# Kernel optimization log

Hardware: AMD Instinct MI355X
Metric: run time of the kernel (lower is better)

Reference implementation:

```python
import jax, jax.numpy as jnp
import numpy as np

D_IN = 1024
D_OUT = 1024
N, S = 4, 2048

def setup_inputs() -> dict:
    key = jax.random.key(0)
    kv, kk, kq, k1, k2, k3 = jax.random.split(key, 6)
    return {
        "v": jax.random.normal(kv, (N, S, D_IN), dtype=jnp.float32),
        "k": jax.random.normal(kk, (N, S, D_IN), dtype=jnp.float32),
        "q": jax.random.normal(kq, (N, S, D_IN), dtype=jnp.float32),
        "WV": jax.random.normal(k1, (D_OUT, D_IN), dtype=jnp.float32),
        "WQ": jax.random.normal(k2, (D_OUT, D_IN), dtype=jnp.float32),
        "WK": jax.random.normal(k3, (D_OUT, D_IN), dtype=jnp.float32),
    }

def reference(v, k, q, WV, WQ, WK) -> jnp.ndarray:
    # projections: x @ W.T  -> [N, S, D_OUT]
    wv = jnp.einsum('nsw,ow->nso', v, WV)
    wk = jnp.einsum('nsw,ow->nso', k, WK)
    wq = jnp.einsum('nsw,ow->nso', q, WQ)
    # scores [N, Sq, Sk]; NOTE: softmax over axis=1 (query axis, matching torch dim=1),
    # then post-hoc division by input_shape[0] AFTER softmax (faithful to source).
    scores = jnp.einsum('nqo,nko->nqk', wq, wk)
    wqk = jax.nn.softmax(scores, axis=1) / jnp.float32(D_IN)
    return jnp.einsum('nqk,nko->nqo', wqk, wv)
```

## Files before the change

### kernel.cpp

```cpp
#include <hip/hip_runtime.h>
#include <math.h>


typedef _Float16 f16;
typedef _Float16 f16x8 __attribute__((ext_vector_type(8)));
typedef _Float16 f16x4 __attribute__((ext_vector_type(4)));
typedef float f32x4 __attribute__((ext_vector_type(4)));

enum StageMode { SM_PLANES2, SM_PLANES1 };
enum EpiMode   { EPI_F32, EPI_SPLIT, EPI_F16T };

#define GLL_PITCH 32

__device__ __forceinline__ void gll16(const f16* g, f16* l) {
    __builtin_amdgcn_global_load_lds(
        (const __attribute__((address_space(1))) void*)g,
        (__attribute__((address_space(3))) void*)l, 16, 0, 0);
}

__device__ __forceinline__ void stage_gll_plane(const f16* __restrict__ gplane,
                                                f16* __restrict__ lds,
                                                long rowBase, int ld, int k0,
                                                int wave, int lane)
{
#pragma unroll
    for (int i = 0; i < 2; i++) {
        int slotBase = (wave * 2 + i) * 64;
        int t = slotBase + lane;
        int r = t >> 2;
        int c = (t & 3) ^ ((r >> 1) & 3);
        const f16* g = gplane + (rowBase + r) * (long)ld + k0 + c * 8;
        gll16(g, lds + (long)slotBase * 8);
    }
}

__device__ __forceinline__ int frag_off_gll(int row, int g) {
    return row * GLL_PITCH + ((g ^ ((row >> 1) & 3)) << 3);
}

template<StageMode SA, StageMode SB, EpiMode EP, int GROUPM, bool STATS>
__global__ __launch_bounds__(256, 4)
void mfma_gemm(const f16* __restrict__ Ahi, const f16* __restrict__ Alo,
               const f16* __restrict__ Bhi, const f16* __restrict__ Blo,
               float* __restrict__ pmOut, float* __restrict__ psOut,
               void* __restrict__ C0, void* __restrict__ C1,
               int M, int Nc, int K, int lda, int ldb, int ldc,
               long batchA, long batchB, long batchC,
               float epiScale, int tsShift)
{
    constexpr bool TRIPLE = (SA == SM_PLANES2);
    constexpr int PLANE_SZ = 128 * GLL_PITCH;

    int bx, by;
    if constexpr (GROUPM > 0) {
        int gx = gridDim.x;
        int lin = blockIdx.y * gx + blockIdx.x;
        int nig = GROUPM * gx;
        int gid = lin / nig;
        int rem = lin - gid * nig;
        by = gid * GROUPM + (rem % GROUPM);
        bx = rem / GROUPM;
    } else {
        bx = blockIdx.x;
        by = blockIdx.y;
    }
    const int n0 = bx * 128;
    const int m0 = by * 128;
    const long z = blockIdx.z;

    const long aOfs = z * batchA, bOfs = z * batchB, cOfs = z * batchC;

    __shared__ __align__(16) f16 As_hi[PLANE_SZ];
    __shared__ __align__(16) f16 Bs_hi[PLANE_SZ];
    __shared__ __align__(16) f16 As_lo[TRIPLE ? PLANE_SZ : 8];
    __shared__ __align__(16) f16 Bs_lo[TRIPLE ? PLANE_SZ : 8];

    const int tid  = threadIdx.x;
    const int lane = tid & 63;
    const int wave = tid >> 6;
    const int wr = (wave >> 1) * 64;
    const int wc = (wave & 1) * 64;
    const int fm = lane & 15;
    const int fg = lane >> 4;

    f32x4 acc[4][4];
#pragma unroll
    for (int i = 0; i < 4; i++)
#pragma unroll
        for (int j = 0; j < 4; j++) acc[i][j] = (f32x4){0.f, 0.f, 0.f, 0.f};

    int roA[4], roB[4];
#pragma unroll
    for (int i = 0; i < 4; i++) {
        roA[i] = frag_off_gll(wr + i * 16 + fm, fg);
        roB[i] = frag_off_gll(wc + i * 16 + fm, fg);
    }

    for (int k0 = 0; k0 < K; k0 += 32) {
        stage_gll_plane(Ahi + aOfs, As_hi, m0, lda, k0, wave, lane);
        stage_gll_plane(Bhi + bOfs, Bs_hi, n0, ldb, k0, wave, lane);
        if constexpr (TRIPLE) {
            stage_gll_plane(Alo + aOfs, As_lo, m0, lda, k0, wave, lane);
            stage_gll_plane(Blo + bOfs, Bs_lo, n0, ldb, k0, wave, lane);
        }
        __syncthreads();

        f16x8 ah[4], bh[4], al[4], bl[4];
#pragma unroll
        for (int i = 0; i < 4; i++) {
            ah[i] = *(const f16x8*)&As_hi[roA[i]];
            bh[i] = *(const f16x8*)&Bs_hi[roB[i]];
            if constexpr (TRIPLE) {
                al[i] = *(const f16x8*)&As_lo[roA[i]];
                bl[i] = *(const f16x8*)&Bs_lo[roB[i]];
            }
        }
#pragma unroll
        for (int i = 0; i < 4; i++) {
#pragma unroll
            for (int j = 0; j < 4; j++) {
                acc[i][j] = __builtin_amdgcn_mfma_f32_16x16x32_f16(ah[i], bh[j], acc[i][j], 0, 0, 0);
                if constexpr (TRIPLE) {
                    acc[i][j] = __builtin_amdgcn_mfma_f32_16x16x32_f16(ah[i], bl[j], acc[i][j], 0, 0, 0);
                    acc[i][j] = __builtin_amdgcn_mfma_f32_16x16x32_f16(al[i], bh[j], acc[i][j], 0, 0, 0);
                }
            }
        }
        __syncthreads();
    }

    const int cr = fg * 4;
    const int cn = fm;
#pragma unroll
    for (int i = 0; i < 4; i++) {
#pragma unroll
        for (int j = 0; j < 4; j++) {
#pragma unroll
            for (int r = 0; r < 4; r++) {
                long mg = m0 + wr + i * 16 + cr + r;
                long ng = n0 + wc + j * 16 + cn;
                float val = acc[i][j][r] * epiScale;
                if constexpr (EP == EPI_F32) {
                    ((float*)C0)[cOfs + mg * ldc + ng] = val;
                } else if constexpr (EP == EPI_SPLIT) {
                    f16 h = (f16)val;
                    ((f16*)C0)[cOfs + mg * ldc + ng] = h;
                    ((f16*)C1)[cOfs + mg * ldc + ng] = (f16)(val - (float)h);
                } else {
                    long TS = 1L << tsShift;
                    long nb = mg >> tsShift;
                    long s  = mg & (TS - 1);
                    long addr = nb * ((long)Nc << tsShift) + ng * TS + s;
                    ((f16*)C0)[addr] = (f16)val;
                }
            }
        }
    }

    if constexpr (STATS) {
        __shared__ float stM[2][128];
        __shared__ float stS[2][128];
#pragma unroll
        for (int j = 0; j < 4; j++) {
            float mj = -3.402823466e38f;
#pragma unroll
            for (int i = 0; i < 4; i++)
#pragma unroll
                for (int r = 0; r < 4; r++) mj = fmaxf(mj, acc[i][j][r]);
            float sj = 0.f;
#pragma unroll
            for (int i = 0; i < 4; i++)
#pragma unroll
                for (int r = 0; r < 4; r++) sj += __expf(acc[i][j][r] - mj);
#pragma unroll
            for (int mask = 16; mask <= 32; mask <<= 1) {
                float mo = __shfl_xor(mj, mask, 64);
                float so = __shfl_xor(sj, mask, 64);
                float mn = fmaxf(mj, mo);
                sj = sj * __expf(mj - mn) + so * __expf(mo - mn);
                mj = mn;
            }
            if (fg == 0) {
                stM[wave >> 1][wc + j * 16 + cn] = mj;
                stS[wave >> 1][wc + j * 16 + cn] = sj;
            }
        }
        __syncthreads();
        if (tid < 128) {
            float ma = stM[0][tid], mb = stM[1][tid];
            float Mc = fmaxf(ma, mb);
            float Sv = stS[0][tid] * __expf(ma - Mc) + stS[1][tid] * __expf(mb - Mc);
            long o = ((long)z * (M >> 7) + by) * (long)Nc + (long)bx * 128 + tid;
            pmOut[o] = Mc;
            psOut[o] = Sv;
        }
    }
}

template<bool HAS_LO>
__global__ __launch_bounds__(256)
void split_kernel(const float* __restrict__ src, f16* __restrict__ hi,
                  f16* __restrict__ lo, long n)
{
    long i = ((long)blockIdx.x * 256 + threadIdx.x) * 8;
    if (i >= n) return;
    float4 x0 = *(const float4*)&src[i];
    float4 x1 = *(const float4*)&src[i + 4];
    float xs[8] = {x0.x, x0.y, x0.z, x0.w, x1.x, x1.y, x1.z, x1.w};
    f16x8 h, l;
#pragma unroll
    for (int e = 0; e < 8; e++) {
        f16 hh = (f16)xs[e];
        h[e] = hh;
        if (HAS_LO) l[e] = (f16)(xs[e] - (float)hh);
    }
    *(f16x8*)&hi[i] = h;
    if (HAS_LO) *(f16x8*)&lo[i] = l;
}

__global__ __launch_bounds__(64)
void stats_combine_kernel(const float* __restrict__ pm, const float* __restrict__ ps,
                          float* __restrict__ statM, float* __restrict__ statR, int S)
{
    const int n = blockIdx.y;
    const int kk = blockIdx.x * 64 + threadIdx.x;
    float M = -INFINITY;
#pragma unroll
    for (int i = 0; i < 16; i++)
        M = fmaxf(M, pm[((long)n * 16 + i) * S + kk]);
    float Ssum = 0.f;
#pragma unroll
    for (int i = 0; i < 16; i++)
        Ssum += ps[((long)n * 16 + i) * S + kk] * __expf(pm[((long)n * 16 + i) * S + kk] - M);
    statM[(long)n * S + kk] = M;
    statR[(long)n * S + kk] = 1.0f / Ssum;
}

__global__ __launch_bounds__(256)
void pmat_kernel(const float* __restrict__ Sc, const float* __restrict__ statM,
                 const float* __restrict__ statR, f16* __restrict__ Phi, int S)
{
    const int n = blockIdx.z;
    const int kk = blockIdx.x * 1024 + threadIdx.x * 4;
    const float* Sn = Sc + (long)n * S * S;
    f16* ph = Phi + (long)n * S * S;
    float4 M4 = *(const float4*)&statM[(long)n * S + kk];
    float4 R4 = *(const float4*)&statR[(long)n * S + kk];
    const int q0 = blockIdx.y * 32;
    for (int qi = 0; qi < 32; qi++) {
        long idx = (long)(q0 + qi) * S + kk;
        float4 x = *(const float4*)&Sn[idx];
        f16x4 p;
        p[0] = (f16)(__expf(x.x - M4.x) * R4.x);
        p[1] = (f16)(__expf(x.y - M4.y) * R4.y);
        p[2] = (f16)(__expf(x.z - M4.z) * R4.z);
        p[3] = (f16)(__expf(x.w - M4.w) * R4.w);
        *(f16x4*)&ph[idx] = p;
    }
}

extern "C" void kernel_launch(void* const* d_in, const int* in_sizes, int n_in,
                              void* d_out, int out_size, void* d_ws, size_t ws_size,
                              hipStream_t stream)
{
    const float* v  = (const float*)d_in[0];
    const float* k  = (const float*)d_in[1];
    const float* q  = (const float*)d_in[2];
    const float* WV = (const float*)d_in[3];
    const float* WQ = (const float*)d_in[4];
    const float* WK = (const float*)d_in[5];
    float* out = (float*)d_out;

    const int N = 4, S = 2048, D = 1024;
    const long NSD = (long)N * S * D;
    const long DD  = (long)D * D;

    f16* ws = (f16*)d_ws;
    f16* q_hi = ws;
    f16* q_lo = ws + NSD;
    f16* k_hi = ws + 2 * NSD;
    f16* k_lo = ws + 3 * NSD;
    f16* v_hi = ws + 4 * NSD;
    f16* Wb   = ws + 5 * NSD;
    f16* WQ_hi = Wb,          *WQ_lo = Wb + DD;
    f16* WK_hi = Wb + 2 * DD, *WK_lo = Wb + 3 * DD;
    f16* WV_hi = Wb + 4 * DD;
    f16* wq_hi = ws + 5 * NSD + 5 * DD;
    f16* wq_lo = wq_hi + NSD;
    f16* wk_hi = wq_hi + 2 * NSD;
    f16* wk_lo = wq_hi + 3 * NSD;
    f16* wvT_hi = ws;
    float* Sc   = (float*)(ws + NSD);
    f16* P_hi   = wq_hi;
    float* pm    = (float*)(ws + 9 * NSD + 5 * DD);
    float* ps    = pm + (long)N * 16 * S;
    float* statM = ps + (long)N * 16 * S;
    float* statR = statM + (long)N * S;

    dim3 blk(256);

    split_kernel<true ><<<dim3(NSD / 2048), blk, 0, stream>>>(q,  q_hi, q_lo, NSD);
    split_kernel<true ><<<dim3(NSD / 2048), blk, 0, stream>>>(k,  k_hi, k_lo, NSD);
    split_kernel<false><<<dim3(NSD / 2048), blk, 0, stream>>>(v,  v_hi, nullptr, NSD);
    split_kernel<true ><<<dim3(DD / 2048),  blk, 0, stream>>>(WQ, WQ_hi, WQ_lo, DD);
    split_kernel<true ><<<dim3(DD / 2048),  blk, 0, stream>>>(WK, WK_hi, WK_lo, DD);
    split_kernel<false><<<dim3(DD / 2048),  blk, 0, stream>>>(WV, WV_hi, nullptr, DD);

    {
        dim3 g(D / 128, (N * S) / 128, 1);
        mfma_gemm<SM_PLANES2, SM_PLANES2, EPI_SPLIT, 4, false><<<g, blk, 0, stream>>>(
            q_hi, q_lo, WQ_hi, WQ_lo, nullptr, nullptr, wq_hi, wq_lo,
            N * S, D, D, D, D, D, 0, 0, 0, 1.0f, 0);
        mfma_gemm<SM_PLANES2, SM_PLANES2, EPI_SPLIT, 4, false><<<g, blk, 0, stream>>>(
            k_hi, k_lo, WK_hi, WK_lo, nullptr, nullptr, wk_hi, wk_lo,
            N * S, D, D, D, D, D, 0, 0, 0, 1.0f, 0);
        mfma_gemm<SM_PLANES1, SM_PLANES1, EPI_F16T, 4, false><<<g, blk, 0, stream>>>(
            v_hi, nullptr, WV_hi, nullptr, nullptr, nullptr, wvT_hi, nullptr,
            N * S, D, D, D, D, 0, 0, 0, 0, 1.0f, 11 );
    }
    {
        dim3 g(S / 128, S / 128, N);
        mfma_gemm<SM_PLANES2, SM_PLANES2, EPI_F32, 4, true><<<g, blk, 0, stream>>>(
            wq_hi, wq_lo, wk_hi, wk_lo, pm, ps, Sc, nullptr,
            S, S, D, D, D, S, (long)S * D, (long)S * D, (long)S * S, 1.0f, 0);
    }
    {
        dim3 gB(S / 64, N);
        stats_combine_kernel<<<gB, dim3(64), 0, stream>>>(pm, ps, statM, statR, S);
    }
    {
        dim3 g(S / 1024, S / 32, N);
        pmat_kernel<<<g, blk, 0, stream>>>(Sc, statM, statR, P_hi, S);
    }
    {
        dim3 g(D / 128, S / 128, N);
        mfma_gemm<SM_PLANES1, SM_PLANES1, EPI_F32, 4, false><<<g, blk, 0, stream>>>(
            P_hi, nullptr, wvT_hi, nullptr, nullptr, nullptr, out, nullptr,
            S, D, S, S, S, D, (long)S * S, (long)S * D, (long)S * D, 1.0f / (float)D, 0);
    }
}
```

Baseline: 471.8 us.

## Fuse softmax normalization into PV GEMM A-load and merge split kernels

Removes the separate pmat kernel by having the final GEMM stage fp32 scores into LDS and apply exp(x-M)*R with an f16 conversion in registers while building A fragments. This avoids writing and re-reading the f16 probability matrix, but each of the 8 column tiles now rereads fp32 scores and recomputes the exponentials. The six split launches are also merged into two launches. The fused GEMM uses launch bounds of 2 blocks and no group swizzle, because of the larger LDS footprint and register use.

```diff
diff --git a/kernel.cpp b/kernel.cpp
--- a/kernel.cpp
+++ b/kernel.cpp
@@ -4,15 +4,14 @@
 
 typedef _Float16 f16;
 typedef _Float16 f16x8 __attribute__((ext_vector_type(8)));
-typedef _Float16 f16x4 __attribute__((ext_vector_type(4)));
 typedef float f32x4 __attribute__((ext_vector_type(4)));
 
-enum StageMode { SM_PLANES2, SM_PLANES1 };
+enum StageMode { SM_PLANES2, SM_PLANES1, SM_EXPF32 };
 enum EpiMode   { EPI_F32, EPI_SPLIT, EPI_F16T };
 
 #define GLL_PITCH 32
 
-__device__ __forceinline__ void gll16(const f16* g, f16* l) {
+__device__ __forceinline__ void gll16(const void* g, void* l) {
     __builtin_amdgcn_global_load_lds(
         (const __attribute__((address_space(1))) void*)g,
         (__attribute__((address_space(3))) void*)l, 16, 0, 0);
@@ -34,14 +33,31 @@
     }
 }
 
+__device__ __forceinline__ void stage_gll_f32(const float* __restrict__ gplane,
+                                              float* __restrict__ lds,
+                                              long rowBase, int ld, int k0,
+                                              int wave, int lane)
+{
+#pragma unroll
+    for (int i = 0; i < 4; i++) {
+        int slotBase = (wave * 4 + i) * 64;
+        int t = slotBase + lane;
+        int r = t >> 3;
+        int lc = (t & 7) ^ (r & 7);
+        const float* g = gplane + (rowBase + r) * (long)ld + k0 + lc * 4;
+        gll16(g, lds + (long)slotBase * 4);
+    }
+}
+
 __device__ __forceinline__ int frag_off_gll(int row, int g) {
     return row * GLL_PITCH + ((g ^ ((row >> 1) & 3)) << 3);
 }
 
-template<StageMode SA, StageMode SB, EpiMode EP, int GROUPM, bool STATS>
-__global__ __launch_bounds__(256, 4)
-void mfma_gemm(const f16* __restrict__ Ahi, const f16* __restrict__ Alo,
-               const f16* __restrict__ Bhi, const f16* __restrict__ Blo,
+template<StageMode SA, StageMode SB, EpiMode EP, int GROUPM, bool STATS, int LB>
+__global__ __launch_bounds__(256, LB)
+void mfma_gemm(const void* __restrict__ Ahi, const void* __restrict__ Alo,
+               const void* __restrict__ Bhi, const void* __restrict__ Blo,
+               const float* __restrict__ statM, const float* __restrict__ statR,
                float* __restrict__ pmOut, float* __restrict__ psOut,
                void* __restrict__ C0, void* __restrict__ C1,
                int M, int Nc, int K, int lda, int ldb, int ldc,
@@ -50,6 +66,7 @@
 {
     constexpr bool TRIPLE = (SA == SM_PLANES2);
     constexpr int PLANE_SZ = 128 * GLL_PITCH;
+    constexpr bool A_F32 = (SA == SM_EXPF32);
 
     int bx, by;
     if constexpr (GROUPM > 0) {
@@ -70,7 +87,7 @@
 
     const long aOfs = z * batchA, bOfs = z * batchB, cOfs = z * batchC;
 
-    __shared__ __align__(16) f16 As_hi[PLANE_SZ];
+    __shared__ __align__(16) f16 As_hi[A_F32 ? 2 * PLANE_SZ : PLANE_SZ];
     __shared__ __align__(16) f16 Bs_hi[PLANE_SZ];
     __shared__ __align__(16) f16 As_lo[TRIPLE ? PLANE_SZ : 8];
     __shared__ __align__(16) f16 Bs_lo[TRIPLE ? PLANE_SZ : 8];
@@ -97,23 +114,55 @@
     }
 
     for (int k0 = 0; k0 < K; k0 += 32) {
-        stage_gll_plane(Ahi + aOfs, As_hi, m0, lda, k0, wave, lane);
-        stage_gll_plane(Bhi + bOfs, Bs_hi, n0, ldb, k0, wave, lane);
-        if constexpr (TRIPLE) {
-            stage_gll_plane(Alo + aOfs, As_lo, m0, lda, k0, wave, lane);
-            stage_gll_plane(Blo + bOfs, Bs_lo, n0, ldb, k0, wave, lane);
-        }
+        if constexpr (A_F32) {
+            stage_gll_f32((const float*)Ahi + aOfs, (float*)As_hi, m0, lda, k0, wave, lane);
+        } else {
+            stage_gll_plane((const f16*)Ahi + aOfs, As_hi, m0, lda, k0, wave, lane);
+            if constexpr (TRIPLE)
+                stage_gll_plane((const f16*)Alo + aOfs, As_lo, m0, lda, k0, wave, lane);
+        }
+        stage_gll_plane((const f16*)Bhi + bOfs, Bs_hi, n0, ldb, k0, wave, lane);
+        if constexpr (TRIPLE)
+            stage_gll_plane((const f16*)Blo + bOfs, Bs_lo, n0, ldb, k0, wave, lane);
         __syncthreads();
 
         f16x8 ah[4], bh[4], al[4], bl[4];
+        if constexpr (A_F32) {
+            const float* pM = statM + z * (long)K;
+            const float* pR = statR + z * (long)K;
+            float4 Ma = *(const float4*)&pM[k0 + fg * 8];
+            float4 Mb = *(const float4*)&pM[k0 + fg * 8 + 4];
+            float4 Ra = *(const float4*)&pR[k0 + fg * 8];
+            float4 Rb = *(const float4*)&pR[k0 + fg * 8 + 4];
+            const float* Asf = (const float*)As_hi;
+            const int p0 = (fg << 1) ^ (fm & 7);
+#pragma unroll
+            for (int i = 0; i < 4; i++) {
+                int ra = wr + i * 16 + fm;
+                float4 xa = *(const float4*)&Asf[ra * 32 + p0 * 4];
+                float4 xb = *(const float4*)&Asf[ra * 32 + (p0 ^ 1) * 4];
+                f16x8 h;
+                h[0] = (f16)(__expf(xa.x - Ma.x) * Ra.x);
+                h[1] = (f16)(__expf(xa.y - Ma.y) * Ra.y);
+                h[2] = (f16)(__expf(xa.z - Ma.z) * Ra.z);
+                h[3] = (f16)(__expf(xa.w - Ma.w) * Ra.w);
+                h[4] = (f16)(__expf(xb.x - Mb.x) * Rb.x);
+                h[5] = (f16)(__expf(xb.y - Mb.y) * Rb.y);
+                h[6] = (f16)(__expf(xb.z - Mb.z) * Rb.z);
+                h[7] = (f16)(__expf(xb.w - Mb.w) * Rb.w);
+                ah[i] = h;
+            }
+        } else {
+#pragma unroll
+            for (int i = 0; i < 4; i++) {
+                ah[i] = *(const f16x8*)&As_hi[roA[i]];
+                if constexpr (TRIPLE) al[i] = *(const f16x8*)&As_lo[roA[i]];
+            }
+        }
 #pragma unroll
         for (int i = 0; i < 4; i++) {
-            ah[i] = *(const f16x8*)&As_hi[roA[i]];
             bh[i] = *(const f16x8*)&Bs_hi[roB[i]];
-            if constexpr (TRIPLE) {
-                al[i] = *(const f16x8*)&As_lo[roA[i]];
-                bl[i] = *(const f16x8*)&Bs_lo[roB[i]];
-            }
+            if constexpr (TRIPLE) bl[i] = *(const f16x8*)&Bs_lo[roB[i]];
         }
 #pragma unroll
         for (int i = 0; i < 4; i++) {
@@ -197,11 +246,17 @@
     }
 }
 
-template<bool HAS_LO>
 __global__ __launch_bounds__(256)
-void split_kernel(const float* __restrict__ src, f16* __restrict__ hi,
-                  f16* __restrict__ lo, long n)
-{
+void split3_kernel(const float* __restrict__ s0, const float* __restrict__ s1,
+                   const float* __restrict__ s2,
+                   f16* __restrict__ h0, f16* __restrict__ l0,
+                   f16* __restrict__ h1, f16* __restrict__ l1,
+                   f16* __restrict__ h2, long n)
+{
+    const int which = blockIdx.y;
+    const float* src = which == 0 ? s0 : which == 1 ? s1 : s2;
+    f16* hi = which == 0 ? h0 : which == 1 ? h1 : h2;
+    f16* lo = which == 0 ? l0 : which == 1 ? l1 : nullptr;
     long i = ((long)blockIdx.x * 256 + threadIdx.x) * 8;
     if (i >= n) return;
     float4 x0 = *(const float4*)&src[i];
@@ -212,10 +267,10 @@
     for (int e = 0; e < 8; e++) {
         f16 hh = (f16)xs[e];
         h[e] = hh;
-        if (HAS_LO) l[e] = (f16)(xs[e] - (float)hh);
+        l[e] = (f16)(xs[e] - (float)hh);
     }
     *(f16x8*)&hi[i] = h;
-    if (HAS_LO) *(f16x8*)&lo[i] = l;
+    if (lo) *(f16x8*)&lo[i] = l;
 }
 
 __global__ __launch_bounds__(64)
@@ -234,29 +289,6 @@
         Ssum += ps[((long)n * 16 + i) * S + kk] * __expf(pm[((long)n * 16 + i) * S + kk] - M);
     statM[(long)n * S + kk] = M;
     statR[(long)n * S + kk] = 1.0f / Ssum;
-}
-
-__global__ __launch_bounds__(256)
-void pmat_kernel(const float* __restrict__ Sc, const float* __restrict__ statM,
-                 const float* __restrict__ statR, f16* __restrict__ Phi, int S)
-{
-    const int n = blockIdx.z;
-    const int kk = blockIdx.x * 1024 + threadIdx.x * 4;
-    const float* Sn = Sc + (long)n * S * S;
-    f16* ph = Phi + (long)n * S * S;
-    float4 M4 = *(const float4*)&statM[(long)n * S + kk];
-    float4 R4 = *(const float4*)&statR[(long)n * S + kk];
-    const int q0 = blockIdx.y * 32;
-    for (int qi = 0; qi < 32; qi++) {
-        long idx = (long)(q0 + qi) * S + kk;
-        float4 x = *(const float4*)&Sn[idx];
-        f16x4 p;
-        p[0] = (f16)(__expf(x.x - M4.x) * R4.x);
-        p[1] = (f16)(__expf(x.y - M4.y) * R4.y);
-        p[2] = (f16)(__expf(x.z - M4.z) * R4.z);
-        p[3] = (f16)(__expf(x.w - M4.w) * R4.w);
-        *(f16x4*)&ph[idx] = p;
-    }
 }
 
 extern "C" void kernel_launch(void* const* d_in, const int* in_sizes, int n_in,
@@ -291,7 +323,6 @@
     f16* wk_lo = wq_hi + 3 * NSD;
     f16* wvT_hi = ws;
     float* Sc   = (float*)(ws + NSD);
-    f16* P_hi   = wq_hi;
     float* pm    = (float*)(ws + 9 * NSD + 5 * DD);
     float* ps    = pm + (long)N * 16 * S;
     float* statM = ps + (long)N * 16 * S;
@@ -299,29 +330,27 @@
 
     dim3 blk(256);
 
-    split_kernel<true ><<<dim3(NSD / 2048), blk, 0, stream>>>(q,  q_hi, q_lo, NSD);
-    split_kernel<true ><<<dim3(NSD / 2048), blk, 0, stream>>>(k,  k_hi, k_lo, NSD);
-    split_kernel<false><<<dim3(NSD / 2048), blk, 0, stream>>>(v,  v_hi, nullptr, NSD);
-    split_kernel<true ><<<dim3(DD / 2048),  blk, 0, stream>>>(WQ, WQ_hi, WQ_lo, DD);
-    split_kernel<true ><<<dim3(DD / 2048),  blk, 0, stream>>>(WK, WK_hi, WK_lo, DD);
-    split_kernel<false><<<dim3(DD / 2048),  blk, 0, stream>>>(WV, WV_hi, nullptr, DD);
+    split3_kernel<<<dim3(NSD / 2048, 3), blk, 0, stream>>>(
+        q, k, v, q_hi, q_lo, k_hi, k_lo, v_hi, NSD);
+    split3_kernel<<<dim3(DD / 2048, 3), blk, 0, stream>>>(
+        WQ, WK, WV, WQ_hi, WQ_lo, WK_hi, WK_lo, WV_hi, DD);
 
     {
         dim3 g(D / 128, (N * S) / 128, 1);
-        mfma_gemm<SM_PLANES2, SM_PLANES2, EPI_SPLIT, 4, false><<<g, blk, 0, stream>>>(
-            q_hi, q_lo, WQ_hi, WQ_lo, nullptr, nullptr, wq_hi, wq_lo,
+        mfma_gemm<SM_PLANES2, SM_PLANES2, EPI_SPLIT, 4, false, 4><<<g, blk, 0, stream>>>(
+            q_hi, q_lo, WQ_hi, WQ_lo, nullptr, nullptr, nullptr, nullptr, wq_hi, wq_lo,
             N * S, D, D, D, D, D, 0, 0, 0, 1.0f, 0);
-        mfma_gemm<SM_PLANES2, SM_PLANES2, EPI_SPLIT, 4, false><<<g, blk, 0, stream>>>(
-            k_hi, k_lo, WK_hi, WK_lo, nullptr, nullptr, wk_hi, wk_lo,
+        mfma_gemm<SM_PLANES2, SM_PLANES2, EPI_SPLIT, 4, false, 4><<<g, blk, 0, stream>>>(
+            k_hi, k_lo, WK_hi, WK_lo, nullptr, nullptr, nullptr, nullptr, wk_hi, wk_lo,
             N * S, D, D, D, D, D, 0, 0, 0, 1.0f, 0);
-        mfma_gemm<SM_PLANES1, SM_PLANES1, EPI_F16T, 4, false><<<g, blk, 0, stream>>>(
-            v_hi, nullptr, WV_hi, nullptr, nullptr, nullptr, wvT_hi, nullptr,
+        mfma_gemm<SM_PLANES1, SM_PLANES1, EPI_F16T, 4, false, 4><<<g, blk, 0, stream>>>(
+            v_hi, nullptr, WV_hi, nullptr, nullptr, nullptr, nullptr, nullptr, wvT_hi, nullptr,
             N * S, D, D, D, D, 0, 0, 0, 0, 1.0f, 11 );
     }
     {
         dim3 g(S / 128, S / 128, N);
-        mfma_gemm<SM_PLANES2, SM_PLANES2, EPI_F32, 4, true><<<g, blk, 0, stream>>>(
-            wq_hi, wq_lo, wk_hi, wk_lo, pm, ps, Sc, nullptr,
+        mfma_gemm<SM_PLANES2, SM_PLANES2, EPI_F32, 4, true, 4><<<g, blk, 0, stream>>>(
+            wq_hi, wq_lo, wk_hi, wk_lo, nullptr, nullptr, pm, ps, Sc, nullptr,
             S, S, D, D, D, S, (long)S * D, (long)S * D, (long)S * S, 1.0f, 0);
     }
     {
@@ -329,13 +358,9 @@
         stats_combine_kernel<<<gB, dim3(64), 0, stream>>>(pm, ps, statM, statR, S);
     }
     {
-        dim3 g(S / 1024, S / 32, N);
-        pmat_kernel<<<g, blk, 0, stream>>>(Sc, statM, statR, P_hi, S);
-    }
-    {
         dim3 g(D / 128, S / 128, N);
-        mfma_gemm<SM_PLANES1, SM_PLANES1, EPI_F32, 4, false><<<g, blk, 0, stream>>>(
-            P_hi, nullptr, wvT_hi, nullptr, nullptr, nullptr, out, nullptr,
+        mfma_gemm<SM_EXPF32, SM_PLANES1, EPI_F32, 0, false, 2><<<g, blk, 0, stream>>>(
+            Sc, nullptr, wvT_hi, nullptr, statM, statR, nullptr, nullptr, out, nullptr,
             S, D, S, S, S, D, (long)S * S, (long)S * D, (long)S * D, 1.0f / (float)D, 0);
     }
 }
```

Result: slower. 510.6 us (+8.2%).
